# Kernel optimization log

Hardware: AMD Instinct MI355X
Metric: run time of the kernel (lower is better)

## Reference

```python
import jax, jax.numpy as jnp
import numpy as np

DIM = 768
HEADS = 12
HEAD_DIM = DIM // HEADS
HIDDEN = 4 * DIM
EPS = 1e-5


def _ln(x, w, b):
    mu = jnp.mean(x, axis=-1, keepdims=True)
    var = jnp.var(x, axis=-1, keepdims=True)
    return (x - mu) * jax.lax.rsqrt(var + EPS) * w + b


def setup_inputs() -> dict:
    key = jax.random.key(0)
    ks = jax.random.split(key, 8)
    B, N, C = 8, 1024, DIM
    s = 0.02
    return {
        "before": jax.random.normal(ks[0], (B, N, C), jnp.float32),
        "after": jax.random.normal(ks[1], (B, N, C), jnp.float32),
        "norm1_w": jnp.ones((C,), jnp.float32),
        "norm1_b": jnp.zeros((C,), jnp.float32),
        "qkv_w": jax.random.normal(ks[2], (3 * C, C), jnp.float32) * s,
        "hln_w": jnp.ones((HEAD_DIM,), jnp.float32),
        "hln_b": jnp.zeros((HEAD_DIM,), jnp.float32),
        "proj_w": jax.random.normal(ks[3], (C, C), jnp.float32) * s,
        "proj_b": jnp.zeros((C,), jnp.float32),
        "norm2_w": jnp.ones((C,), jnp.float32),
        "norm2_b": jnp.zeros((C,), jnp.float32),
        "fc1_w": jax.random.normal(ks[4], (HIDDEN, C), jnp.float32) * s,
        "fc1_b": jnp.zeros((HIDDEN,), jnp.float32),
        "fc2_w": jax.random.normal(ks[5], (C, HIDDEN), jnp.float32) * s,
        "fc2_b": jnp.zeros((C,), jnp.float32),
    }


def _qkv_normed(x, qkv_w, hln_w, hln_b):
    B, N, C = x.shape
    qkv = x @ qkv_w.T  # (B,N,3C)
    qkv = qkv.reshape(B, N, 3, HEADS, HEAD_DIM).transpose(2, 0, 3, 1, 4)  # (3,B,H,N,hd)
    qkv = _ln(qkv, hln_w, hln_b)  # per-head LayerNorm over head_dim
    return qkv[0], qkv[1], qkv[2]


def _cross_attn(q, k, v, proj_w, proj_b):
    B, H, N, D = q.shape
    scale = D ** (-0.5)
    attn = jax.nn.softmax(jnp.einsum("bhnd,bhmd->bhnm", q, k) * scale, axis=-1)
    ctx = jnp.einsum("bhnm,bhmd->bhnd", attn, v)
    ctx = ctx.transpose(0, 2, 1, 3).reshape(B, N, H * D)
    ctx = ctx @ proj_w.T + proj_b
    # NOTE: original adds q.reshape(B,N,C) WITHOUT transposing heads (faithful)
    return ctx + q.reshape(B, N, H * D)


def _mlp(x, fc1_w, fc1_b, fc2_w, fc2_b):
    h = jax.nn.gelu(x @ fc1_w.T + fc1_b, approximate=False)
    return h @ fc2_w.T + fc2_b


def reference(before, after, norm1_w, norm1_b, qkv_w, hln_w, hln_b, proj_w, proj_b,
              norm2_w, norm2_b, fc1_w, fc1_b, fc2_w, fc2_b):
    before_n = _ln(before, norm1_w, norm1_b)
    after_n = _ln(after, norm1_w, norm1_b)
    q_b, k_b, v_b = _qkv_normed(before_n, qkv_w, hln_w, hln_b)
    q_a, k_a, v_a = _qkv_normed(after_n, qkv_w, hln_w, hln_b)
    context_a = _cross_attn(q_b, k_a, v_a, proj_w, proj_b)  # before attends to after
    context_b = _cross_attn(q_a, k_b, v_b, proj_w, proj_b)  # after attends to before
    before_o = before_n + context_b
    after_o = after_n + context_a
    before_o = before_o + _mlp(_ln(before_o, norm2_w, norm2_b), fc1_w, fc1_b, fc2_w, fc2_b)
    after_o = after_o + _mlp(_ln(after_o, norm2_w, norm2_b), fc1_w, fc1_b, fc2_w, fc2_b)
    return (before_o, after_o)
```

## Files before the change

### kernel.cpp

```cpp
#include <hip/hip_runtime.h>
#include <hip/hip_bf16.h>

typedef unsigned short u16;
typedef __attribute__((ext_vector_type(8))) short bf16x8;
typedef __attribute__((ext_vector_type(4))) float f32x4;

#define DIRSTRIDE 6291456

__device__ __forceinline__ u16 f2bf(float x){
  __hip_bfloat16 h = __float2bfloat16(x);
  return *reinterpret_cast<u16*>(&h);
}
__device__ __forceinline__ float bf2f(u16 u){
  return __uint_as_float(((unsigned int)u) << 16);
}

__global__ __launch_bounds__(256) void zero_kernel(float* __restrict__ p, int n){
  int i = blockIdx.x*256 + threadIdx.x;
  if (i < n) p[i] = 0.f;
}

__global__ __launch_bounds__(256) void cvt_kernel(const float* __restrict__ s,
                                                  u16* __restrict__ d, int n){
  int i = blockIdx.x*256 + threadIdx.x;
  if (i < n) d[i] = f2bf(s[i]);
}

__global__ __launch_bounds__(256) void ln_kernel(const float* __restrict__ s0,
    const float* __restrict__ s1, const float* __restrict__ w,
    const float* __restrict__ b, u16* __restrict__ out,
    float* __restrict__ mu_out, float* __restrict__ rs_out){
  int r = blockIdx.x;
  const float* src = (r < 8192) ? (s0 + (size_t)r*768) : (s1 + (size_t)(r-8192)*768);
  int t = threadIdx.x;
  float v0 = src[t], v1 = src[t+256], v2 = src[t+512];
  __shared__ float red[4];
  float s = v0+v1+v2;
  #pragma unroll
  for (int o=32;o;o>>=1) s += __shfl_xor(s,o);
  if ((t&63)==0) red[t>>6] = s;
  __syncthreads();
  float mean = (red[0]+red[1]+red[2]+red[3]) * (1.0f/768.0f);
  float d0=v0-mean, d1=v1-mean, d2=v2-mean;
  float q = d0*d0+d1*d1+d2*d2;
  __syncthreads();
  #pragma unroll
  for (int o=32;o;o>>=1) q += __shfl_xor(q,o);
  if ((t&63)==0) red[t>>6] = q;
  __syncthreads();
  float var = (red[0]+red[1]+red[2]+red[3]) * (1.0f/768.0f);
  float rstd = rsqrtf(var + 1e-5f);
  if (mu_out && t == 0){ mu_out[r] = mean; rs_out[r] = rstd; }
  size_t base = (size_t)r*768;
  out[base+t]     = f2bf(d0*rstd*w[t]     + b[t]);
  out[base+t+256] = f2bf(d1*rstd*w[t+256] + b[t+256]);
  out[base+t+512] = f2bf(d2*rstd*w[t+512] + b[t+512]);
}

__device__ __forceinline__ void stage_tile64(const u16* g, size_t strideK, u16* lds,
                                             int w, int lane){
  #pragma unroll
  for (int i=0;i<4;i++){
    int row = w*32 + i*8 + (lane>>3);
    int cs  = (lane&7) ^ (row&7);
    const u16* gp = g + (size_t)row*strideK + cs*8;
    __builtin_amdgcn_global_load_lds(
        (const __attribute__((address_space(1))) unsigned int*)gp,
        (__attribute__((address_space(3))) unsigned int*)(lds + (w*4+i)*512),
        16, 0, 0);
  }
}

#define SWZ_FRAG(tile, r, c) (*(const bf16x8*)&(tile)[(r)*64 + (((c) ^ ((r)&7)))*8])

template<int EPI>
__global__ __launch_bounds__(256, 4) void gemm_kernel(
    const u16* __restrict__ A, const u16* __restrict__ W, void* Cout,
    const float* __restrict__ bias, const float* resF,
    int M, int N, int K)
{
  __shared__ __attribute__((aligned(16))) u16 sA[128*64];
  __shared__ __attribute__((aligned(16))) u16 sB[128*64];
  int t = threadIdx.x;
  int w = t>>6, lane = t&63, ln = lane&15, quad = lane>>4;
  int m0 = blockIdx.y*128, n0 = blockIdx.x*128;
  int wr = (w>>1)*64, wc = (w&1)*64;
  f32x4 acc[4][4];
  #pragma unroll
  for (int mi=0;mi<4;mi++)
    #pragma unroll
    for (int ni=0;ni<4;ni++) acc[mi][ni] = (f32x4){0.f,0.f,0.f,0.f};
  int KB = K >> 6;
  for (int kb=0;kb<KB;kb++){
    __syncthreads();
    stage_tile64(A + (size_t)m0*K + kb*64, K, sA, w, lane);
    stage_tile64(W + (size_t)n0*K + kb*64, K, sB, w, lane);
    __syncthreads();
    #pragma unroll
    for (int ks=0;ks<2;ks++){
      bf16x8 aF[4], bF[4];
      #pragma unroll
      for (int mi=0;mi<4;mi++) aF[mi] = SWZ_FRAG(sA, wr+mi*16+ln, ks*4+quad);
      #pragma unroll
      for (int ni=0;ni<4;ni++) bF[ni] = SWZ_FRAG(sB, wc+ni*16+ln, ks*4+quad);
      #pragma unroll
      for (int mi=0;mi<4;mi++)
        #pragma unroll
        for (int ni=0;ni<4;ni++)
          acc[mi][ni] = __builtin_amdgcn_mfma_f32_16x16x32_bf16(aF[mi], bF[ni], acc[mi][ni], 0,0,0);
    }
  }
  #pragma unroll
  for (int mi=0;mi<4;mi++){
    #pragma unroll
    for (int ni=0;ni<4;ni++){
      #pragma unroll
      for (int r=0;r<4;r++){
        int row = m0 + wr + mi*16 + quad*4 + r;
        int col = n0 + wc + ni*16 + ln;
        size_t ridx = (size_t)row*N + col;
        float v = acc[mi][ni][r];
        if (EPI == 2){
          v += bias[col];
          v = 0.5f*v*(1.0f + erff(v*0.70710678118654752f));
          ((u16*)Cout)[ridx] = f2bf(v);
        } else {
          float rf = resF[ridx];
          ((float*)Cout)[ridx] = v + bias[col] + rf;
        }
      }
    }
  }
}

__global__ __launch_bounds__(256, 4) void gemm_proj_kernel(
    const u16* __restrict__ A, const u16* __restrict__ W, float* Cout,
    const float* __restrict__ bias, const u16* __restrict__ resQ,
    const float* __restrict__ before, const float* __restrict__ after,
    const float* __restrict__ n1w, const float* __restrict__ n1b,
    const float* __restrict__ mu, const float* __restrict__ rstd)
{
  const int K = 768, N = 768, KB = 12;
  __shared__ __attribute__((aligned(16))) u16 sA[128*64];
  __shared__ __attribute__((aligned(16))) u16 sB[128*64];
  int t = threadIdx.x;
  int w = t>>6, lane = t&63, ln = lane&15, quad = lane>>4;
  int m0 = blockIdx.y*128, n0 = blockIdx.x*128;
  int wr = (w>>1)*64, wc = (w&1)*64;
  f32x4 acc[4][4];
  #pragma unroll
  for (int mi=0;mi<4;mi++)
    #pragma unroll
    for (int ni=0;ni<4;ni++) acc[mi][ni] = (f32x4){0.f,0.f,0.f,0.f};
  for (int kb=0;kb<KB;kb++){
    __syncthreads();
    stage_tile64(A + (size_t)m0*K + kb*64, K, sA, w, lane);
    stage_tile64(W + (size_t)n0*K + kb*64, K, sB, w, lane);
    __syncthreads();
    #pragma unroll
    for (int ks=0;ks<2;ks++){
      bf16x8 aF[4], bF[4];
      #pragma unroll
      for (int mi=0;mi<4;mi++) aF[mi] = SWZ_FRAG(sA, wr+mi*16+ln, ks*4+quad);
      #pragma unroll
      for (int ni=0;ni<4;ni++) bF[ni] = SWZ_FRAG(sB, wc+ni*16+ln, ks*4+quad);
      #pragma unroll
      for (int mi=0;mi<4;mi++)
        #pragma unroll
        for (int ni=0;ni<4;ni++)
          acc[mi][ni] = __builtin_amdgcn_mfma_f32_16x16x32_bf16(aF[mi], bF[ni], acc[mi][ni], 0,0,0);
    }
  }
  #pragma unroll
  for (int mi=0;mi<4;mi++){
    #pragma unroll
    for (int ni=0;ni<4;ni++){
      #pragma unroll
      for (int r=0;r<4;r++){
        int row = m0 + wr + mi*16 + quad*4 + r;
        int col = n0 + wc + ni*16 + ln;
        size_t ridx = (size_t)row*N + col;
        int dirout = row >> 13;
        int rem = row & 8191;
        size_t qidx = (size_t)(1-dirout)*DIRSTRIDE + (size_t)rem*768 + col;
        const float* src = dirout ? after : before;
        float xr = (src[(size_t)rem*768 + col] - mu[row]) * rstd[row] * n1w[col] + n1b[col];
        Cout[ridx] = acc[mi][ni][r] + bias[col] + bf2f(resQ[qidx]) + xr;
      }
    }
  }
}

__global__ __launch_bounds__(256, 4) void gemm_qkv_kernel(
    const u16* __restrict__ A, const u16* __restrict__ W,
    const float* __restrict__ hw, const float* __restrict__ hb,
    u16* __restrict__ q, u16* __restrict__ k, u16* __restrict__ vt)
{
  const int K = 768, KB = 12;
  __shared__ __attribute__((aligned(16))) u16 sA[128*64];
  __shared__ __attribute__((aligned(16))) u16 sB[128*64];
  int t = threadIdx.x;
  int w = t>>6, lane = t&63, ln = lane&15, quad = lane>>4;
  int m0 = blockIdx.y*128, n0 = blockIdx.x*128;
  int wr = (w>>1)*64, wc = (w&1)*64;
  f32x4 acc[4][4];
  #pragma unroll
  for (int mi=0;mi<4;mi++)
    #pragma unroll
    for (int ni=0;ni<4;ni++) acc[mi][ni] = (f32x4){0.f,0.f,0.f,0.f};
  for (int kb=0;kb<KB;kb++){
    __syncthreads();
    stage_tile64(A + (size_t)m0*K + kb*64, K, sA, w, lane);
    stage_tile64(W + (size_t)n0*K + kb*64, K, sB, w, lane);
    __syncthreads();
    #pragma unroll
    for (int ks=0;ks<2;ks++){
      bf16x8 aF[4], bF[4];
      #pragma unroll
      for (int mi=0;mi<4;mi++) aF[mi] = SWZ_FRAG(sA, wr+mi*16+ln, ks*4+quad);
      #pragma unroll
      for (int ni=0;ni<4;ni++) bF[ni] = SWZ_FRAG(sB, wc+ni*16+ln, ks*4+quad);
      #pragma unroll
      for (int mi=0;mi<4;mi++)
        #pragma unroll
        for (int ni=0;ni<4;ni++)
          acc[mi][ni] = __builtin_amdgcn_mfma_f32_16x16x32_bf16(aF[mi], bF[ni], acc[mi][ni], 0,0,0);
    }
  }
  int sec = (n0 + wc) >> 6;
  int which = sec / 12, h = sec - which*12;
  float hwv[4], hbv[4];
  #pragma unroll
  for (int ni=0;ni<4;ni++){ hwv[ni] = hw[ni*16+ln]; hbv[ni] = hb[ni*16+ln]; }
  #pragma unroll
  for (int mi=0;mi<4;mi++){
    #pragma unroll
    for (int r=0;r<4;r++){
      float s = acc[mi][0][r]+acc[mi][1][r]+acc[mi][2][r]+acc[mi][3][r];
      #pragma unroll
      for (int ofs=1; ofs<16; ofs<<=1) s += __shfl_xor(s, ofs);
      float mu = s * (1.0f/64.0f);
      float vv = 0.f;
      #pragma unroll
      for (int ni=0;ni<4;ni++){ float d = acc[mi][ni][r]-mu; vv += d*d; }
      #pragma unroll
      for (int ofs=1; ofs<16; ofs<<=1) vv += __shfl_xor(vv, ofs);
      float rstd = rsqrtf(vv*(1.0f/64.0f) + 1e-5f);
      int token = m0 + wr + mi*16 + quad*4 + r;
      int dir = token >> 13, bb = (token>>10)&7, n = token & 1023;
      size_t base = (size_t)dir*DIRSTRIDE + (size_t)bb*786432 + (size_t)h*65536;
      #pragma unroll
      for (int ni=0;ni<4;ni++){
        u16 y = f2bf((acc[mi][ni][r]-mu)*rstd*hwv[ni] + hbv[ni]);
        int hd = ni*16 + ln;
        if (which == 0)      q[base + (size_t)n*64 + hd] = y;
        else if (which == 1) k[base + (size_t)n*64 + hd] = y;
        else                 vt[base + (size_t)hd*1024 + n] = y;
      }
    }
  }
}

__global__ __launch_bounds__(256) void flash_kernel(const u16* __restrict__ qg,
    const u16* __restrict__ kg, const u16* __restrict__ vtg, u16* __restrict__ ctx)
{
  __shared__ __attribute__((aligned(16))) u16 sK[64*72];
  __shared__ __attribute__((aligned(16))) u16 sV[64*72];
  __shared__ __attribute__((aligned(16))) u16 sP[4*16*72];
  int qt = blockIdx.x, bh = blockIdx.y, dout = blockIdx.z;
  int b = bh/12, h = bh - b*12;
  size_t qbase = (size_t)(1-dout)*DIRSTRIDE + (size_t)b*786432 + (size_t)h*65536;
  size_t kbase = (size_t)dout*DIRSTRIDE + (size_t)b*786432 + (size_t)h*65536;
  int t = threadIdx.x;
  int w = t>>6, lane = t&63, ln = lane&15, quad = lane>>4;
  const u16* qp = qg + qbase + (size_t)(qt*64 + w*16 + ln)*64 + quad*8;
  bf16x8 aQ0 = *(const bf16x8*)qp;
  bf16x8 aQ1 = *(const bf16x8*)(qp + 32);
  bf16x8 vOne;
  #pragma unroll
  for (int j=0;j<8;j++) vOne[j] = (short)0x3F80;
  f32x4 o[4];
  #pragma unroll
  for (int ni=0;ni<4;ni++) o[ni] = (f32x4){0.f,0.f,0.f,0.f};
  f32x4 oL = (f32x4){0.f,0.f,0.f,0.f};
  u16* pw = &sP[w*16*72];
  const float cs = 0.18033688011112042f;
  for (int kt=0;kt<16;kt++){
    __syncthreads();
    #pragma unroll
    for (int i=0;i<2;i++){
      int idx = t + (i<<8);
      int row = idx>>3, c8 = (idx&7)<<3;
      *(uint4*)&sK[row*72 + c8] = *(const uint4*)&kg[kbase + (size_t)(kt*64+row)*64 + c8];
      *(uint4*)&sV[row*72 + c8] = *(const uint4*)&vtg[kbase + (size_t)row*1024 + kt*64 + c8];
    }
    __syncthreads();
    f32x4 s[4];
    #pragma unroll
    for (int ni=0;ni<4;ni++){
      bf16x8 bK0 = *(const bf16x8*)&sK[(ni*16+ln)*72 + quad*8];
      bf16x8 bK1 = *(const bf16x8*)&sK[(ni*16+ln)*72 + 32 + quad*8];
      s[ni] = (f32x4){0.f,0.f,0.f,0.f};
      s[ni] = __builtin_amdgcn_mfma_f32_16x16x32_bf16(aQ0, bK0, s[ni], 0,0,0);
      s[ni] = __builtin_amdgcn_mfma_f32_16x16x32_bf16(aQ1, bK1, s[ni], 0,0,0);
    }
    bf16x8 bV[4][2];
    #pragma unroll
    for (int ni=0;ni<4;ni++){
      bV[ni][0] = *(const bf16x8*)&sV[(ni*16+ln)*72 + quad*8];
      bV[ni][1] = *(const bf16x8*)&sV[(ni*16+ln)*72 + 32 + quad*8];
    }
    #pragma unroll
    for (int ni=0;ni<4;ni++){
      #pragma unroll
      for (int r=0;r<4;r++){
        float p = exp2f(fminf(fmaxf(s[ni][r]*cs, -30.f), 30.f));
        pw[(quad*4+r)*72 + ni*16 + ln] = f2bf(p);
      }
    }
    __syncthreads();
    bf16x8 aP0 = *(const bf16x8*)&pw[ln*72 + quad*8];
    bf16x8 aP1 = *(const bf16x8*)&pw[ln*72 + 32 + quad*8];
    #pragma unroll
    for (int ni=0;ni<4;ni++){
      o[ni] = __builtin_amdgcn_mfma_f32_16x16x32_bf16(aP0, bV[ni][0], o[ni], 0,0,0);
      o[ni] = __builtin_amdgcn_mfma_f32_16x16x32_bf16(aP1, bV[ni][1], o[ni], 0,0,0);
    }
    oL = __builtin_amdgcn_mfma_f32_16x16x32_bf16(aP0, vOne, oL, 0,0,0);
    oL = __builtin_amdgcn_mfma_f32_16x16x32_bf16(aP1, vOne, oL, 0,0,0);
  }
  #pragma unroll
  for (int ni=0;ni<4;ni++){
    #pragma unroll
    for (int r=0;r<4;r++){
      int row = qt*64 + w*16 + quad*4 + r;
      float val = o[ni][r] / oL[r];
      ctx[((size_t)dout*8192 + (size_t)b*1024 + row)*768 + h*64 + ni*16 + ln] = f2bf(val);
    }
  }
}

extern "C" void kernel_launch(void* const* d_in, const int* in_sizes, int n_in,
                              void* d_out, int out_size, void* d_ws, size_t ws_size,
                              hipStream_t stream)
{
  const float* before = (const float*)d_in[0];
  const float* after  = (const float*)d_in[1];
  const float* n1w  = (const float*)d_in[2];
  const float* n1b  = (const float*)d_in[3];
  const float* qkvw = (const float*)d_in[4];
  const float* hlnw = (const float*)d_in[5];
  const float* hlnb = (const float*)d_in[6];
  const float* projw= (const float*)d_in[7];
  const float* projb= (const float*)d_in[8];
  const float* n2w  = (const float*)d_in[9];
  const float* n2b  = (const float*)d_in[10];
  const float* fc1w = (const float*)d_in[11];
  const float* fc1b = (const float*)d_in[12];
  const float* fc2w = (const float*)d_in[13];
  const float* fc2b = (const float*)d_in[14];

  const size_t REQUIRED = 114950144;
  if (ws_size < REQUIRED){
    zero_kernel<<<(out_size + 255)/256, 256, 0, stream>>>((float*)d_out, out_size);
    return;
  }

  char* ws = (char*)d_ws;
  u16* xn    = (u16*)(ws + 0);
  u16* ctxb  = (u16*)(ws + 0);
  u16* gbuf  = (u16*)(ws + 0);
  u16* qb    = (u16*)(ws + 25165824);
  u16* kb    = (u16*)(ws + 50331648);
  u16* h1n   = (u16*)(ws + 50331648);
  u16* vtb   = (u16*)(ws + 75497472);
  u16* wqkv  = (u16*)(ws + 100663296);
  u16* wproj = (u16*)(ws + 104202240);
  u16* wfc1  = (u16*)(ws + 105381888);
  u16* wfc2  = (u16*)(ws + 110100480);
  float* mu1  = (float*)(ws + 114819072);
  float* rs1  = (float*)(ws + 114884608);
  float* h1   = (float*)d_out;
  float* outp = (float*)d_out;

  cvt_kernel<<<6912, 256, 0, stream>>>(qkvw, wqkv, 1769472);
  cvt_kernel<<<2304, 256, 0, stream>>>(projw, wproj, 589824);
  cvt_kernel<<<9216, 256, 0, stream>>>(fc1w, wfc1, 2359296);
  cvt_kernel<<<9216, 256, 0, stream>>>(fc2w, wfc2, 2359296);

  ln_kernel<<<16384, 256, 0, stream>>>(before, after, n1w, n1b, xn, mu1, rs1);
  gemm_qkv_kernel<<<dim3(18,128), 256, 0, stream>>>(xn, wqkv, hlnw, hlnb, qb, kb, vtb);
  flash_kernel<<<dim3(16,96,2), 256, 0, stream>>>(qb, kb, vtb, ctxb);
  gemm_proj_kernel<<<dim3(6,128), 256, 0, stream>>>(ctxb, wproj, h1,
      projb, qb, before, after, n1w, n1b, mu1, rs1);
  ln_kernel<<<16384, 256, 0, stream>>>(h1, h1 + (size_t)8192*768, n2w, n2b, h1n,
      nullptr, nullptr);
  for (int c = 0; c < 2; c++){
    size_t off = (size_t)c * 8192 * 768;
    gemm_kernel<2><<<dim3(24,64), 256, 0, stream>>>(h1n + off, wfc1, gbuf,
        fc1b, nullptr, 8192, 3072, 768);
    gemm_kernel<3><<<dim3(6,64), 256, 0, stream>>>(gbuf, wfc2, outp + off,
        fc2b, h1 + off, 8192, 768, 3072);
  }
}
```

Before: 703.7 us.

## Load K/V fragments directly from global in flash kernel, drop LDS staging

Each wave in the flash attention kernel now loads its K and V^T MFMA operand fragments straight from global memory into registers, replacing the shared-memory staging and the block-wide barriers around it. The block index is remapped so that groups of eight consecutive blocks cover different heads and directions, aiming for better cache locality across XCDs. s_setprio is raised around the MFMA sections. Each of the four waves now re-reads the same K/V tiles from global or L2 instead of sharing one LDS copy, which adds memory traffic in exchange for removing the syncs. Dropping the barrier before reading P is safe because each wave only reads its own slice of sP, and a wave's LDS operations stay in order.

```diff
diff --git a/kernel.cpp b/kernel.cpp
--- a/kernel.cpp
+++ b/kernel.cpp
@@ -264,10 +264,12 @@
 __global__ __launch_bounds__(256) void flash_kernel(const u16* __restrict__ qg,
     const u16* __restrict__ kg, const u16* __restrict__ vtg, u16* __restrict__ ctx)
 {
-  __shared__ __attribute__((aligned(16))) u16 sK[64*72];
-  __shared__ __attribute__((aligned(16))) u16 sV[64*72];
   __shared__ __attribute__((aligned(16))) u16 sP[4*16*72];
-  int qt = blockIdx.x, bh = blockIdx.y, dout = blockIdx.z;
+  int lin = (int)blockIdx.x + 16*((int)blockIdx.y + 96*(int)blockIdx.z);
+  int x8 = lin & 7, jj = lin >> 3;
+  int qt = jj & 15;
+  int g  = x8 + 8*(jj >> 4);
+  int dout = g & 1, bh = g >> 1;
   int b = bh/12, h = bh - b*12;
   size_t qbase = (size_t)(1-dout)*DIRSTRIDE + (size_t)b*786432 + (size_t)h*65536;
   size_t kbase = (size_t)dout*DIRSTRIDE + (size_t)b*786432 + (size_t)h*65536;
@@ -276,6 +278,8 @@
   const u16* qp = qg + qbase + (size_t)(qt*64 + w*16 + ln)*64 + quad*8;
   bf16x8 aQ0 = *(const bf16x8*)qp;
   bf16x8 aQ1 = *(const bf16x8*)(qp + 32);
+  const u16* kp = kg  + kbase + (size_t)ln*64   + quad*8;
+  const u16* vp = vtg + kbase + (size_t)ln*1024 + quad*8;
   bf16x8 vOne;
   #pragma unroll
   for (int j=0;j<8;j++) vOne[j] = (short)0x3F80;
@@ -286,30 +290,29 @@
   u16* pw = &sP[w*16*72];
   const float cs = 0.18033688011112042f;
   for (int kt=0;kt<16;kt++){
-    __syncthreads();
-    #pragma unroll
-    for (int i=0;i<2;i++){
-      int idx = t + (i<<8);
-      int row = idx>>3, c8 = (idx&7)<<3;
-      *(uint4*)&sK[row*72 + c8] = *(const uint4*)&kg[kbase + (size_t)(kt*64+row)*64 + c8];
-      *(uint4*)&sV[row*72 + c8] = *(const uint4*)&vtg[kbase + (size_t)row*1024 + kt*64 + c8];
-    }
-    __syncthreads();
+    bf16x8 bK[4][2];
+    #pragma unroll
+    for (int ni=0;ni<4;ni++){
+      const u16* kr = kp + (size_t)((kt*64 + ni*16))*64;
+      bK[ni][0] = *(const bf16x8*)kr;
+      bK[ni][1] = *(const bf16x8*)(kr + 32);
+    }
+    bf16x8 bV[4][2];
+    #pragma unroll
+    for (int ni=0;ni<4;ni++){
+      const u16* vr = vp + (size_t)(ni*16)*1024 + kt*64;
+      bV[ni][0] = *(const bf16x8*)vr;
+      bV[ni][1] = *(const bf16x8*)(vr + 32);
+    }
     f32x4 s[4];
-    #pragma unroll
-    for (int ni=0;ni<4;ni++){
-      bf16x8 bK0 = *(const bf16x8*)&sK[(ni*16+ln)*72 + quad*8];
-      bf16x8 bK1 = *(const bf16x8*)&sK[(ni*16+ln)*72 + 32 + quad*8];
+    __builtin_amdgcn_s_setprio(1);
+    #pragma unroll
+    for (int ni=0;ni<4;ni++){
       s[ni] = (f32x4){0.f,0.f,0.f,0.f};
-      s[ni] = __builtin_amdgcn_mfma_f32_16x16x32_bf16(aQ0, bK0, s[ni], 0,0,0);
-      s[ni] = __builtin_amdgcn_mfma_f32_16x16x32_bf16(aQ1, bK1, s[ni], 0,0,0);
-    }
-    bf16x8 bV[4][2];
-    #pragma unroll
-    for (int ni=0;ni<4;ni++){
-      bV[ni][0] = *(const bf16x8*)&sV[(ni*16+ln)*72 + quad*8];
-      bV[ni][1] = *(const bf16x8*)&sV[(ni*16+ln)*72 + 32 + quad*8];
-    }
+      s[ni] = __builtin_amdgcn_mfma_f32_16x16x32_bf16(aQ0, bK[ni][0], s[ni], 0,0,0);
+      s[ni] = __builtin_amdgcn_mfma_f32_16x16x32_bf16(aQ1, bK[ni][1], s[ni], 0,0,0);
+    }
+    __builtin_amdgcn_s_setprio(0);
     #pragma unroll
     for (int ni=0;ni<4;ni++){
       #pragma unroll
@@ -318,9 +321,9 @@
         pw[(quad*4+r)*72 + ni*16 + ln] = f2bf(p);
       }
     }
-    __syncthreads();
     bf16x8 aP0 = *(const bf16x8*)&pw[ln*72 + quad*8];
     bf16x8 aP1 = *(const bf16x8*)&pw[ln*72 + 32 + quad*8];
+    __builtin_amdgcn_s_setprio(1);
     #pragma unroll
     for (int ni=0;ni<4;ni++){
       o[ni] = __builtin_amdgcn_mfma_f32_16x16x32_bf16(aP0, bV[ni][0], o[ni], 0,0,0);
@@ -328,6 +331,7 @@
     }
     oL = __builtin_amdgcn_mfma_f32_16x16x32_bf16(aP0, vOne, oL, 0,0,0);
     oL = __builtin_amdgcn_mfma_f32_16x16x32_bf16(aP1, vOne, oL, 0,0,0);
+    __builtin_amdgcn_s_setprio(0);
   }
   #pragma unroll
   for (int ni=0;ni<4;ni++){
```

New measurement: 981.8 us. 39.5% more time.
